# Kernel optimization log

Measured on AMD Instinct MI355X. Metric: run time of the kernel, lower is better.

Reference implementation:

```python
import jax, jax.numpy as jnp
import numpy as np

N_NODES = 100000


def _mean_aggregate(h, src, dst, inv_deg):
    # gather source-node features per edge, scatter-add into dst, divide by in-degree
    summed = jax.ops.segment_sum(h[src], dst, num_segments=N_NODES)  # [N, d]
    return summed * inv_deg[:, None]


def setup_inputs() -> dict:
    key = jax.random.key(0)
    ks = jax.random.split(key, 6)
    n_edges, d = 640000, 128
    h = jax.random.normal(ks[0], (N_NODES, d), dtype=jnp.float32)
    src = jax.random.randint(ks[1], (n_edges,), 0, N_NODES, dtype=jnp.int64)
    dst = jax.random.randint(ks[2], (n_edges,), 0, N_NODES, dtype=jnp.int64)
    W_self = jax.random.normal(ks[3], (3, d, d), dtype=jnp.float32) / np.sqrt(d)
    W_neigh = jax.random.normal(ks[4], (3, d, d), dtype=jnp.float32) / np.sqrt(d)
    b = jnp.zeros((3, d), dtype=jnp.float32)
    return {"h": h, "src": src, "dst": dst, "W_self": W_self, "W_neigh": W_neigh, "b": b}


def reference(h, src, dst, W_self, W_neigh, b):
    # in-degree with clamp to 1 (isolated nodes aggregate to zero)
    deg = jax.ops.segment_sum(jnp.ones_like(src, dtype=h.dtype), dst, num_segments=N_NODES)
    inv_deg = 1.0 / jnp.maximum(deg, 1.0)
    n_layers = W_self.shape[0]
    for i in range(n_layers):
        neigh = _mean_aggregate(h, src, dst, inv_deg)
        h = h @ W_self[i] + neigh @ W_neigh[i] + b[i]
        if i < n_layers - 1:
            h = jax.nn.relu(h)  # dropout p=0 / eval: no-op
    return h
```

## Files before the change

### kernel.cpp

```cpp
#include <hip/hip_runtime.h>
#include <cstdint>
#include <cstddef>

#define NN 100000
#define D 128
#define K2 256

typedef __attribute__((ext_vector_type(8))) short bf16x8;
typedef __attribute__((ext_vector_type(4))) float f32x4;

__device__ inline float bfhi2f(unsigned int u) {
    union { unsigned int i; float f; } v; v.i = u & 0xffff0000u; return v.f;
}
__device__ inline float bflo2f(unsigned int u) {
    union { unsigned int i; float f; } v; v.i = u << 16; return v.f;
}
__device__ inline unsigned short f2bf(float f) {
    union { float f; unsigned int i; } v; v.f = f;
    unsigned int r = v.i + 0x7FFFu + ((v.i >> 16) & 1u);
    return (unsigned short)(r >> 16);
}

__global__ void k_deg(const int* __restrict__ dst, int ne, int* __restrict__ deg) {
    int e = blockIdx.x * blockDim.x + threadIdx.x;
    if (e < ne) atomicAdd(&deg[dst[e]], 1);
}

__global__ void k_chunk_reduce(const int* __restrict__ deg, int n, int* __restrict__ bsum) {
    __shared__ int s[256];
    int i = blockIdx.x * 256 + threadIdx.x;
    s[threadIdx.x] = (i < n) ? deg[i] : 0;
    __syncthreads();
    for (int off = 128; off > 0; off >>= 1) {
        if (threadIdx.x < off) s[threadIdx.x] += s[threadIdx.x + off];
        __syncthreads();
    }
    if (threadIdx.x == 0) bsum[blockIdx.x] = s[0];
}

__global__ __launch_bounds__(512) void k_scan_partials(int* __restrict__ bsum, int nb,
                                                       int* __restrict__ rowptr, int n) {
    __shared__ int s[512];
    int tid = threadIdx.x;
    int v = (tid < nb) ? bsum[tid] : 0;
    s[tid] = v;
    __syncthreads();
    for (int off = 1; off < 512; off <<= 1) {
        int t = (tid >= off) ? s[tid - off] : 0;
        __syncthreads();
        s[tid] += t;
        __syncthreads();
    }
    if (tid < nb) bsum[tid] = s[tid] - v;
    if (tid == nb - 1) rowptr[n] = s[tid];
}

__global__ void k_chunk_scan(const int* __restrict__ deg, int n, const int* __restrict__ bsum,
                             int* __restrict__ rowptr, int* __restrict__ cursor,
                             float* __restrict__ invd) {
    __shared__ int s[256];
    int tid = threadIdx.x;
    int i = blockIdx.x * 256 + tid;
    int v = (i < n) ? deg[i] : 0;
    s[tid] = v;
    __syncthreads();
    for (int off = 1; off < 256; off <<= 1) {
        int t = (tid >= off) ? s[tid - off] : 0;
        __syncthreads();
        s[tid] += t;
        __syncthreads();
    }
    if (i < n) {
        int excl = bsum[blockIdx.x] + s[tid] - v;
        rowptr[i] = excl;
        cursor[i] = excl;
        invd[i] = 1.0f / fmaxf((float)v, 1.0f);
    }
}

__global__ void k_fill(const int* __restrict__ src, const int* __restrict__ dst, int ne,
                       int* __restrict__ cursor, int* __restrict__ col) {
    int e = blockIdx.x * blockDim.x + threadIdx.x;
    if (e < ne) {
        int p = atomicAdd(&cursor[dst[e]], 1);
        col[p] = src[e];
    }
}

#define T_H   (NN * 32)
#define T_BT  (3 * 128 * K2)
#define T_Z   (NN / 4)
__global__ void k_prep(const float* __restrict__ h, const float* __restrict__ Ws,
                       const float* __restrict__ Wn, unsigned short* __restrict__ Ht,
                       unsigned short* __restrict__ Btf, int4* __restrict__ degz) {
    int t = blockIdx.x * 256 + threadIdx.x;
    if (t < T_H) {
        int row = t >> 5, c4 = (t & 31) << 2;
        float4 v = *(const float4*)(h + (size_t)row * D + c4);
        ushort4 o = make_ushort4(f2bf(v.x), f2bf(v.y), f2bf(v.z), f2bf(v.w));
        *(ushort4*)(Ht + (size_t)row * D + c4) = o;
    } else if (t < T_H + T_BT) {
        int t2 = t - T_H;
        int j = t2 & 7; int rest = t2 >> 3;
        int lane = rest & 63; rest >>= 6;
        int ks = rest & 7; rest >>= 3;
        int nf = rest & 7; int l = rest >> 3;
        int nn = nf * 16 + (lane & 15);
        int k = ks * 32 + (lane >> 4) * 8 + j;
        float v = (k < D) ? Ws[(size_t)l * D * D + (size_t)k * D + nn]
                          : Wn[(size_t)l * D * D + (size_t)(k - D) * D + nn];
        Btf[t2] = f2bf(v);
    } else {
        int t3 = t - T_H - T_BT;
        if (t3 < T_Z) degz[t3] = make_int4(0, 0, 0, 0);
    }
}

__global__ __launch_bounds__(256) void k_agg(const unsigned short* __restrict__ Ht,
                                             unsigned short* __restrict__ Nt,
                                             const int* __restrict__ rowptr,
                                             const int* __restrict__ col,
                                             const float* __restrict__ invd) {
    int wave = (blockIdx.x * 256 + threadIdx.x) >> 6;
    int lane = threadIdx.x & 63;
    int g = lane >> 4;
    int lane16 = lane & 15;
    int node = wave * 4 + g;
    int e0 = rowptr[node];
    int n = rowptr[node + 1] - e0;
    float inv = invd[node];
    int coff = lane16 * 8;
    float a0 = 0.f, a1 = 0.f, a2 = 0.f, a3 = 0.f, a4 = 0.f, a5 = 0.f, a6 = 0.f, a7 = 0.f;
    for (int base = 0; base < n; base += 16) {
        int rem = n - base;
        int lim = rem < 16 ? rem : 16;
        int cidx = lane16 < rem ? lane16 : rem - 1;
        int cv = col[e0 + base + cidx];
        for (int j = 0; j < lim; j += 8) {
            uint4 u[8];
#pragma unroll
            for (int k = 0; k < 8; ++k) {
                int ee = j + k;
                int eidx = ee < lim ? ee : lim - 1;
                int si = __shfl(cv, (g << 4) + eidx, 64);
                u[k] = *(const uint4*)(Ht + (size_t)si * D + coff);
            }
#pragma unroll
            for (int k = 0; k < 8; ++k) {
                bool live = (j + k) < lim;
                unsigned int ux = live ? u[k].x : 0u, uy = live ? u[k].y : 0u;
                unsigned int uz = live ? u[k].z : 0u, uw = live ? u[k].w : 0u;
                a0 += bflo2f(ux); a1 += bfhi2f(ux);
                a2 += bflo2f(uy); a3 += bfhi2f(uy);
                a4 += bflo2f(uz); a5 += bfhi2f(uz);
                a6 += bflo2f(uw); a7 += bfhi2f(uw);
            }
        }
    }
    uint4 o;
    o.x = ((unsigned int)f2bf(a1 * inv) << 16) | f2bf(a0 * inv);
    o.y = ((unsigned int)f2bf(a3 * inv) << 16) | f2bf(a2 * inv);
    o.z = ((unsigned int)f2bf(a5 * inv) << 16) | f2bf(a4 * inv);
    o.w = ((unsigned int)f2bf(a7 * inv) << 16) | f2bf(a6 * inv);
    *(uint4*)(Nt + (size_t)node * D + coff) = o;
}

__global__ __launch_bounds__(256, 3) void k_gemm(const unsigned short* __restrict__ Ht,
                                                 const unsigned short* __restrict__ Btf,
                                                 const float* __restrict__ bias,
                                                 unsigned short* __restrict__ HtW,
                                                 float* __restrict__ outf,
                                                 int relu, int M) {
    __shared__ unsigned short Alds[64 * K2];
    int wid = threadIdx.x >> 6;
    int lane = threadIdx.x & 63;
    int r16 = lane & 15;
    int g = lane >> 4;
    int m0 = blockIdx.x * 64;

    bf16x8 bfr[2][8];
#pragma unroll
    for (int q = 0; q < 2; ++q) {
        int nf = wid + q * 4;
#pragma unroll
        for (int ks = 0; ks < 8; ++ks)
            bfr[q][ks] = *(const bf16x8*)(Btf + (size_t)(((nf * 8 + ks) << 6) + lane) * 8);
    }

#pragma unroll
    for (int i = 0; i < 8; ++i) {
        int chunk = wid * 8 + i;
        int o = chunk * 1024 + lane * 16;
        int row = o >> 9;
        int half = (o >> 8) & 1;
        int cb = o & 255;
        int scb = cb ^ ((row & 7) << 4);
        const unsigned short* gsrc = Ht + (size_t)(m0 + row) * D + (size_t)half * ((size_t)NN * D) + (scb >> 1);
        __builtin_amdgcn_global_load_lds(
            (const __attribute__((address_space(1))) unsigned int*)gsrc,
            (__attribute__((address_space(3))) unsigned int*)((char*)Alds + chunk * 1024),
            16, 0, 0);
    }
    __syncthreads();

    f32x4 acc[4][2];
#pragma unroll
    for (int mt = 0; mt < 4; ++mt)
#pragma unroll
        for (int q = 0; q < 2; ++q) acc[mt][q] = (f32x4){0.f, 0.f, 0.f, 0.f};

#pragma unroll
    for (int mt = 0; mt < 4; ++mt) {
        int row = mt * 16 + r16;
        bf16x8 a[8];
#pragma unroll
        for (int ks = 0; ks < 8; ++ks) {
            int kb = (ks * 32 + g * 8) * 2;
            int c = kb ^ ((row & 7) << 4);
            a[ks] = *(const bf16x8*)((const char*)Alds + row * 512 + c);
        }
#pragma unroll
        for (int ks = 0; ks < 8; ++ks) {
            acc[mt][0] = __builtin_amdgcn_mfma_f32_16x16x32_bf16(a[ks], bfr[0][ks], acc[mt][0], 0, 0, 0);
            acc[mt][1] = __builtin_amdgcn_mfma_f32_16x16x32_bf16(a[ks], bfr[1][ks], acc[mt][1], 0, 0, 0);
        }
    }

    float bv[2];
    bv[0] = bias[wid * 16 + r16];
    bv[1] = bias[(wid + 4) * 16 + r16];
#pragma unroll
    for (int mt = 0; mt < 4; ++mt) {
#pragma unroll
        for (int q = 0; q < 2; ++q) {
            int colc = (wid + q * 4) * 16 + r16;
#pragma unroll
            for (int i = 0; i < 4; ++i) {
                int row = m0 + mt * 16 + g * 4 + i;
                if (row >= M) continue;
                float v = acc[mt][q][i] + bv[q];
                if (relu) v = fmaxf(v, 0.f);
                if (outf) outf[(size_t)row * D + colc] = v;
                else HtW[(size_t)row * D + colc] = f2bf(v);
            }
        }
    }
}

extern "C" void kernel_launch(void* const* d_in, const int* in_sizes, int n_in,
                              void* d_out, int out_size, void* d_ws, size_t ws_size,
                              hipStream_t stream) {
    const float* h = (const float*)d_in[0];
    const int* src = (const int*)d_in[1];
    const int* dst = (const int*)d_in[2];
    const float* Ws = (const float*)d_in[3];
    const float* Wn = (const float*)d_in[4];
    const float* b = (const float*)d_in[5];
    float* out = (float*)d_out;
    int ne = in_sizes[1];

    char* ws = (char*)d_ws;
    unsigned short* Ht = (unsigned short*)ws; ws += (size_t)NN * D * sizeof(unsigned short);
    unsigned short* Nt = (unsigned short*)ws; ws += (size_t)NN * D * sizeof(unsigned short);
    int* col = (int*)ws;    ws += (size_t)ne * sizeof(int);
    unsigned short* Btf = (unsigned short*)ws; ws += (size_t)3 * 128 * K2 * sizeof(unsigned short);
    int* deg = (int*)ws;    ws += (size_t)NN * sizeof(int);
    int* cursor = (int*)ws; ws += (size_t)NN * sizeof(int);
    int* rowptr = (int*)ws; ws += ((size_t)(NN + 1) * sizeof(int) + 15) / 16 * 16;
    int* bsum = (int*)ws;   ws += 512 * sizeof(int);
    float* invd = (float*)ws;

    int nchunk = (NN + 255) / 256;
    int nprep = (T_H + T_BT + T_Z + 255) / 256;
    k_prep<<<nprep, 256, 0, stream>>>(h, Ws, Wn, Ht, Btf, (int4*)deg);
    k_deg<<<(ne + 255) / 256, 256, 0, stream>>>(dst, ne, deg);
    k_chunk_reduce<<<nchunk, 256, 0, stream>>>(deg, NN, bsum);
    k_scan_partials<<<1, 512, 0, stream>>>(bsum, nchunk, rowptr, NN);
    k_chunk_scan<<<nchunk, 256, 0, stream>>>(deg, NN, bsum, rowptr, cursor, invd);
    k_fill<<<(ne + 255) / 256, 256, 0, stream>>>(src, dst, ne, cursor, col);

    int nagg = (NN / 4 + 3) / 4;
    int ngemm = (NN + 63) / 64;
    for (int layer = 0; layer < 3; ++layer) {
        k_agg<<<nagg, 256, 0, stream>>>(Ht, Nt, rowptr, col, invd);
        k_gemm<<<ngemm, 256, 0, stream>>>(Ht, Btf + (size_t)layer * 128 * K2, b + (size_t)layer * D,
                                          Ht, (layer == 2) ? out : nullptr, (layer < 2) ? 1 : 0, NN);
    }
}
```

Baseline: 231.5 us.

## Fuse neighbor aggregation into the GEMM kernel with ping-pong feature buffers

Merges the per-layer aggregation and GEMM kernels into a single kernel. Each block aggregates neighbor features for its 64 rows straight into shared memory alongside its own rows, then runs the MFMA GEMM, so the aggregated tensor is never written to or re-read from global memory. Two padded feature buffers alternate between layers because in-place updates would race with other blocks' gathers. The cost is that gather latency and MFMA work now share one kernel with lower occupancy (launch bound of 3 blocks), and the two phases no longer overlap across separate kernels.

```diff
diff --git a/kernel.cpp b/kernel.cpp
--- a/kernel.cpp
+++ b/kernel.cpp
@@ -3,6 +3,7 @@
 #include <cstddef>
 
 #define NN 100000
+#define NPAD 100032
 #define D 128
 #define K2 256
 
@@ -116,67 +117,83 @@
     }
 }
 
-__global__ __launch_bounds__(256) void k_agg(const unsigned short* __restrict__ Ht,
-                                             unsigned short* __restrict__ Nt,
-                                             const int* __restrict__ rowptr,
-                                             const int* __restrict__ col,
-                                             const float* __restrict__ invd) {
-    int wave = (blockIdx.x * 256 + threadIdx.x) >> 6;
+__global__ __launch_bounds__(256, 3) void k_layer(const unsigned short* __restrict__ Hin,
+                                                  const unsigned short* __restrict__ Btf,
+                                                  const float* __restrict__ bias,
+                                                  const int* __restrict__ rowptr,
+                                                  const int* __restrict__ col,
+                                                  const float* __restrict__ invd,
+                                                  unsigned short* __restrict__ Hout,
+                                                  float* __restrict__ outf,
+                                                  int relu) {
+    __shared__ unsigned short Ah[64 * 128];
+    __shared__ unsigned short An[64 * 128];
+    int wid = threadIdx.x >> 6;
     int lane = threadIdx.x & 63;
     int g = lane >> 4;
     int lane16 = lane & 15;
-    int node = wave * 4 + g;
-    int e0 = rowptr[node];
-    int n = rowptr[node + 1] - e0;
-    float inv = invd[node];
+    int m0 = blockIdx.x * 64;
+
+#pragma unroll
+    for (int i = 0; i < 4; ++i) {
+        int chunk = wid * 4 + i;
+        int o = chunk * 1024 + lane * 16;
+        int row = o >> 8;
+        int cb = o & 255;
+        int scb = cb ^ ((row & 7) << 4);
+        const unsigned short* gsrc = Hin + (size_t)(m0 + row) * D + (scb >> 1);
+        __builtin_amdgcn_global_load_lds(
+            (const __attribute__((address_space(1))) unsigned int*)gsrc,
+            (__attribute__((address_space(3))) unsigned int*)((char*)Ah + chunk * 1024),
+            16, 0, 0);
+    }
+
     int coff = lane16 * 8;
-    float a0 = 0.f, a1 = 0.f, a2 = 0.f, a3 = 0.f, a4 = 0.f, a5 = 0.f, a6 = 0.f, a7 = 0.f;
-    for (int base = 0; base < n; base += 16) {
-        int rem = n - base;
-        int lim = rem < 16 ? rem : 16;
-        int cidx = lane16 < rem ? lane16 : rem - 1;
-        int cv = col[e0 + base + cidx];
-        for (int j = 0; j < lim; j += 8) {
-            uint4 u[8];
-#pragma unroll
-            for (int k = 0; k < 8; ++k) {
-                int ee = j + k;
-                int eidx = ee < lim ? ee : lim - 1;
-                int si = __shfl(cv, (g << 4) + eidx, 64);
-                u[k] = *(const uint4*)(Ht + (size_t)si * D + coff);
+    for (int c = 0; c < 4; ++c) {
+        int row = wid * 16 + c * 4 + g;
+        int node = m0 + row;
+        int e0 = 0, n = 0;
+        float inv = 0.f;
+        if (node < NN) {
+            e0 = rowptr[node];
+            n = rowptr[node + 1] - e0;
+            inv = invd[node];
+        }
+        float a0 = 0.f, a1 = 0.f, a2 = 0.f, a3 = 0.f, a4 = 0.f, a5 = 0.f, a6 = 0.f, a7 = 0.f;
+        for (int base = 0; base < n; base += 16) {
+            int rem = n - base;
+            int lim = rem < 16 ? rem : 16;
+            int cidx = lane16 < rem ? lane16 : rem - 1;
+            int cv = col[e0 + base + cidx];
+            for (int j = 0; j < lim; j += 8) {
+                uint4 u[8];
+#pragma unroll
+                for (int k = 0; k < 8; ++k) {
+                    int ee = j + k;
+                    int eidx = ee < lim ? ee : lim - 1;
+                    int si = __shfl(cv, (g << 4) + eidx, 64);
+                    u[k] = *(const uint4*)(Hin + (size_t)si * D + coff);
+                }
+#pragma unroll
+                for (int k = 0; k < 8; ++k) {
+                    bool live = (j + k) < lim;
+                    unsigned int ux = live ? u[k].x : 0u, uy = live ? u[k].y : 0u;
+                    unsigned int uz = live ? u[k].z : 0u, uw = live ? u[k].w : 0u;
+                    a0 += bflo2f(ux); a1 += bfhi2f(ux);
+                    a2 += bflo2f(uy); a3 += bfhi2f(uy);
+                    a4 += bflo2f(uz); a5 += bfhi2f(uz);
+                    a6 += bflo2f(uw); a7 += bfhi2f(uw);
+                }
             }
-#pragma unroll
-            for (int k = 0; k < 8; ++k) {
-                bool live = (j + k) < lim;
-                unsigned int ux = live ? u[k].x : 0u, uy = live ? u[k].y : 0u;
-                unsigned int uz = live ? u[k].z : 0u, uw = live ? u[k].w : 0u;
-                a0 += bflo2f(ux); a1 += bfhi2f(ux);
-                a2 += bflo2f(uy); a3 += bfhi2f(uy);
-                a4 += bflo2f(uz); a5 += bfhi2f(uz);
-                a6 += bflo2f(uw); a7 += bfhi2f(uw);
-            }
-        }
-    }
-    uint4 o;
-    o.x = ((unsigned int)f2bf(a1 * inv) << 16) | f2bf(a0 * inv);
-    o.y = ((unsigned int)f2bf(a3 * inv) << 16) | f2bf(a2 * inv);
-    o.z = ((unsigned int)f2bf(a5 * inv) << 16) | f2bf(a4 * inv);
-    o.w = ((unsigned int)f2bf(a7 * inv) << 16) | f2bf(a6 * inv);
-    *(uint4*)(Nt + (size_t)node * D + coff) = o;
-}
-
-__global__ __launch_bounds__(256, 3) void k_gemm(const unsigned short* __restrict__ Ht,
-                                                 const unsigned short* __restrict__ Btf,
-                                                 const float* __restrict__ bias,
-                                                 unsigned short* __restrict__ HtW,
-                                                 float* __restrict__ outf,
-                                                 int relu, int M) {
-    __shared__ unsigned short Alds[64 * K2];
-    int wid = threadIdx.x >> 6;
-    int lane = threadIdx.x & 63;
-    int r16 = lane & 15;
-    int g = lane >> 4;
-    int m0 = blockIdx.x * 64;
+        }
+        uint4 o;
+        o.x = ((unsigned int)f2bf(a1 * inv) << 16) | f2bf(a0 * inv);
+        o.y = ((unsigned int)f2bf(a3 * inv) << 16) | f2bf(a2 * inv);
+        o.z = ((unsigned int)f2bf(a5 * inv) << 16) | f2bf(a4 * inv);
+        o.w = ((unsigned int)f2bf(a7 * inv) << 16) | f2bf(a6 * inv);
+        int bo = row * 256 + ((lane16 * 16) ^ ((row & 7) << 4));
+        *(uint4*)((char*)An + bo) = o;
+    }
 
     bf16x8 bfr[2][8];
 #pragma unroll
@@ -187,20 +204,6 @@
             bfr[q][ks] = *(const bf16x8*)(Btf + (size_t)(((nf * 8 + ks) << 6) + lane) * 8);
     }
 
-#pragma unroll
-    for (int i = 0; i < 8; ++i) {
-        int chunk = wid * 8 + i;
-        int o = chunk * 1024 + lane * 16;
-        int row = o >> 9;
-        int half = (o >> 8) & 1;
-        int cb = o & 255;
-        int scb = cb ^ ((row & 7) << 4);
-        const unsigned short* gsrc = Ht + (size_t)(m0 + row) * D + (size_t)half * ((size_t)NN * D) + (scb >> 1);
-        __builtin_amdgcn_global_load_lds(
-            (const __attribute__((address_space(1))) unsigned int*)gsrc,
-            (__attribute__((address_space(3))) unsigned int*)((char*)Alds + chunk * 1024),
-            16, 0, 0);
-    }
     __syncthreads();
 
     f32x4 acc[4][2];
@@ -211,13 +214,15 @@
 
 #pragma unroll
     for (int mt = 0; mt < 4; ++mt) {
-        int row = mt * 16 + r16;
+        int row = mt * 16 + lane16;
+        int swz = (row & 7) << 4;
         bf16x8 a[8];
 #pragma unroll
         for (int ks = 0; ks < 8; ++ks) {
-            int kb = (ks * 32 + g * 8) * 2;
-            int c = kb ^ ((row & 7) << 4);
-            a[ks] = *(const bf16x8*)((const char*)Alds + row * 512 + c);
+            int kb = ks * 64 + g * 16;
+            const char* basep = (kb < 256) ? (const char*)Ah : (const char*)An;
+            int cb2 = (kb & 255) ^ swz;
+            a[ks] = *(const bf16x8*)(basep + row * 256 + cb2);
         }
 #pragma unroll
         for (int ks = 0; ks < 8; ++ks) {
@@ -227,21 +232,21 @@
     }
 
     float bv[2];
-    bv[0] = bias[wid * 16 + r16];
-    bv[1] = bias[(wid + 4) * 16 + r16];
+    bv[0] = bias[wid * 16 + lane16];
+    bv[1] = bias[(wid + 4) * 16 + lane16];
 #pragma unroll
     for (int mt = 0; mt < 4; ++mt) {
 #pragma unroll
         for (int q = 0; q < 2; ++q) {
-            int colc = (wid + q * 4) * 16 + r16;
+            int colc = (wid + q * 4) * 16 + lane16;
 #pragma unroll
             for (int i = 0; i < 4; ++i) {
                 int row = m0 + mt * 16 + g * 4 + i;
-                if (row >= M) continue;
+                if (row >= NN) continue;
                 float v = acc[mt][q][i] + bv[q];
                 if (relu) v = fmaxf(v, 0.f);
                 if (outf) outf[(size_t)row * D + colc] = v;
-                else HtW[(size_t)row * D + colc] = f2bf(v);
+                else Hout[(size_t)row * D + colc] = f2bf(v);
             }
         }
     }
@@ -260,8 +265,8 @@
     int ne = in_sizes[1];
 
     char* ws = (char*)d_ws;
-    unsigned short* Ht = (unsigned short*)ws; ws += (size_t)NN * D * sizeof(unsigned short);
-    unsigned short* Nt = (unsigned short*)ws; ws += (size_t)NN * D * sizeof(unsigned short);
+    unsigned short* HtA = (unsigned short*)ws; ws += (size_t)NPAD * D * sizeof(unsigned short);
+    unsigned short* HtB = (unsigned short*)ws; ws += (size_t)NPAD * D * sizeof(unsigned short);
     int* col = (int*)ws;    ws += (size_t)ne * sizeof(int);
     unsigned short* Btf = (unsigned short*)ws; ws += (size_t)3 * 128 * K2 * sizeof(unsigned short);
     int* deg = (int*)ws;    ws += (size_t)NN * sizeof(int);
@@ -272,18 +277,18 @@
 
     int nchunk = (NN + 255) / 256;
     int nprep = (T_H + T_BT + T_Z + 255) / 256;
-    k_prep<<<nprep, 256, 0, stream>>>(h, Ws, Wn, Ht, Btf, (int4*)deg);
+    k_prep<<<nprep, 256, 0, stream>>>(h, Ws, Wn, HtA, Btf, (int4*)deg);
     k_deg<<<(ne + 255) / 256, 256, 0, stream>>>(dst, ne, deg);
     k_chunk_reduce<<<nchunk, 256, 0, stream>>>(deg, NN, bsum);
     k_scan_partials<<<1, 512, 0, stream>>>(bsum, nchunk, rowptr, NN);
     k_chunk_scan<<<nchunk, 256, 0, stream>>>(deg, NN, bsum, rowptr, cursor, invd);
     k_fill<<<(ne + 255) / 256, 256, 0, stream>>>(src, dst, ne, cursor, col);
 
-    int nagg = (NN / 4 + 3) / 4;
-    int ngemm = (NN + 63) / 64;
-    for (int layer = 0; layer < 3; ++layer) {
-        k_agg<<<nagg, 256, 0, stream>>>(Ht, Nt, rowptr, col, invd);
-        k_gemm<<<ngemm, 256, 0, stream>>>(Ht, Btf + (size_t)layer * 128 * K2, b + (size_t)layer * D,
-                                          Ht, (layer == 2) ? out : nullptr, (layer < 2) ? 1 : 0, NN);
-    }
-}
+    int ngrid = NPAD / 64;
+    k_layer<<<ngrid, 256, 0, stream>>>(HtA, Btf, b, rowptr, col, invd,
+                                       HtB, nullptr, 1);
+    k_layer<<<ngrid, 256, 0, stream>>>(HtB, Btf + (size_t)1 * 128 * K2, b + 1 * D,
+                                       rowptr, col, invd, HtA, nullptr, 1);
+    k_layer<<<ngrid, 256, 0, stream>>>(HtA, Btf + (size_t)2 * 128 * K2, b + 2 * D,
+                                       rowptr, col, invd, nullptr, out, 0);
+}
```

Measured after the change: 221.2 us. 1.05x faster.
